# Performance work log

Hardware: AMD Instinct MI355X
Metric: run time of the kernel (lower is better)

Reference implementation:

```python
import jax, jax.numpy as jnp
import numpy as np

VOCAB = 10000
EMB = 256
FILTERS = 256
KS = [2, 3, 4]
NUM_LABELS = 6
B, L = 4, 256


def _conv1d_same(x, w, b, k):
    # x: [B, C, L], w: [O, I, k] -> [B, O, L]; torch 'same' pad: left=(k-1)//2
    pad_l = (k - 1) // 2
    pad_r = (k - 1) - pad_l
    y = jax.lax.conv_general_dilated(
        x, w, window_strides=(1,), padding=[(pad_l, pad_r)],
        dimension_numbers=('NCH', 'OIH', 'NCH'))
    return y + b[None, :, None]


def setup_inputs() -> dict:
    key = jax.random.key(0)
    ks = jax.random.split(key, 12)
    s = 0.02
    return {
        'input_ids': jax.random.randint(ks[0], (B, L), 0, VOCAB),
        'emb_table': jax.random.normal(ks[1], (VOCAB, EMB), jnp.float32) * s,
        'w2': jax.random.normal(ks[2], (FILTERS, EMB, 2), jnp.float32) * s,
        'b2': jax.random.normal(ks[3], (FILTERS,), jnp.float32) * s,
        'w3': jax.random.normal(ks[4], (FILTERS, EMB, 3), jnp.float32) * s,
        'b3': jax.random.normal(ks[5], (FILTERS,), jnp.float32) * s,
        'w4': jax.random.normal(ks[6], (FILTERS, EMB, 4), jnp.float32) * s,
        'b4': jax.random.normal(ks[7], (FILTERS,), jnp.float32) * s,
        'triple_w': jax.random.normal(ks[8], (NUM_LABELS, 3 * FILTERS), jnp.float32) * s,
        'triple_b': jax.random.normal(ks[9], (NUM_LABELS,), jnp.float32) * s,
        'score_w': jax.random.normal(ks[10], (1, 3 * FILTERS), jnp.float32) * s,
        'score_b': jax.random.normal(ks[11], (1,), jnp.float32) * s,
    }


def reference(input_ids, emb_table, w2, b2, w3, b3, w4, b4,
              triple_w, triple_b, score_w, score_b):
    emb = emb_table[input_ids]              # [B, L, E]
    x = jnp.transpose(emb, (0, 2, 1))       # [B, E, L]
    outs = [_conv1d_same(x, w, b, k) for (w, b, k)
            in ((w2, b2, 2), (w3, b3, 3), (w4, b4, 4))]
    out = jnp.concatenate(outs, axis=1)     # [B, 3F, L]
    out = jnp.transpose(out, (0, 2, 1))     # [B, L, K], K = 3F
    # dropout is identity in eval mode
    pair = jnp.einsum('bik,bjk->bijk', out, out)          # [B, L, L, K]
    triple_logits = jnp.einsum('bijk,ck->bijc', pair, triple_w) + triple_b
    scores = jnp.einsum('bijk,ck->bijc', pair, score_w) + score_b
    scores = scores[..., 0]                 # squeeze(-1) -> [B, L, L]
    return triple_logits, scores
```

## Files before the change

kernel.cpp:

```cpp
#include <hip/hip_runtime.h>
#include <stdint.h>

#define LSEQ 256
#define EMB  256
#define K3F  768
#define SCOFF (4 * 256 * 256 * 6)

typedef short bf16x8 __attribute__((ext_vector_type(8)));
typedef float f32x4  __attribute__((ext_vector_type(4)));

__device__ __forceinline__ uint16_t f2bf(float x) {
    union { float f; uint32_t u; } c; c.f = x;
    uint32_t r = c.u + 0x7fffu + ((c.u >> 16) & 1u);
    return (uint16_t)(r >> 16);
}

__global__ __launch_bounds__(256) void k_prep(const int* __restrict__ ids,
                                              const float* __restrict__ table,
                                              const float* __restrict__ w2,
                                              const float* __restrict__ w3,
                                              const float* __restrict__ w4,
                                              uint16_t* __restrict__ embB,
                                              uint16_t* __restrict__ Wt2,
                                              uint16_t* __restrict__ Wt3,
                                              uint16_t* __restrict__ Wt4) {
    int blk = blockIdx.x, tid = threadIdx.x;
    if (blk < 32) {
        int b = blk >> 3, l0 = (blk & 7) << 5;
        int r = tid >> 3, p = tid & 7;
        int id = ids[(b << 8) + l0 + r];
        const float* src = table + (size_t)id * EMB + p * 32;
        uint16_t* dst = embB + (size_t)(b * 272 + 4 + l0 + r) * 256 + p * 32;
#pragma unroll
        for (int s = 0; s < 8; ++s) {
            float4 v = *(const float4*)(src + 4 * s);
            uint32_t lo = f2bf(v.x) | ((uint32_t)f2bf(v.y) << 16);
            uint32_t hi = f2bf(v.z) | ((uint32_t)f2bf(v.w) << 16);
            *(uint2*)(dst + 4 * s) = make_uint2(lo, hi);
        }
    } else if (blk < 36) {
        int b = blk - 32;
        int ri = tid >> 4;
        int row = ri < 4 ? ri : 256 + ri;
        int off = (tid & 15) * 16;
        uint16_t* dst = embB + (size_t)(b * 272 + row) * 256 + off;
        *(uint4*)dst = make_uint4(0, 0, 0, 0);
        *(uint4*)(dst + 8) = make_uint4(0, 0, 0, 0);
    } else {
        int n = (blk - 36) * 256 + tid;
        if (n < 131072) {
            int t = n >> 16, rem = n & 65535, c = rem >> 8, i = rem & 255;
            Wt2[n] = f2bf(w2[(c << 9) + (i << 1) + t]);
        } else if (n < 327680) {
            int m = n - 131072;
            int t = m >> 16, rem = m & 65535, c = rem >> 8, i = rem & 255;
            Wt3[m] = f2bf(w3[c * 768 + i * 3 + t]);
        } else if (n < 589824) {
            int m = n - 327680;
            int t = m >> 16, rem = m & 65535, c = rem >> 8, i = rem & 255;
            Wt4[m] = f2bf(w4[(c << 10) + (i << 2) + t]);
        }
    }
}

template <int K, int PAD>
__device__ __forceinline__ void convg_body(const uint16_t* __restrict__ Wt,
                                           const float* __restrict__ bias,
                                           const uint16_t* __restrict__ embB,
                                           const float* __restrict__ tw,
                                           const float* __restrict__ sw,
                                           uint16_t* __restrict__ VB,
                                           uint16_t* __restrict__ U,
                                           int b, int c0, int l0, int gbase,
                                           uint16_t (*As)[32][72], uint16_t (*Bs)[72],
                                           float (*twb)[32]) {
    const int tid = threadIdx.x;
    {
        int cm = tid >> 5, cc = tid & 31;
        int gch = gbase + c0 + cc;
        float v;
        if (cm < 6) v = tw[cm * K3F + gch];
        else if (cm == 6) v = sw[gch];
        else v = bias[c0 + cc];
        twb[cm][cc] = v;
    }
    const int lane = tid & 63, wave = tid >> 6;
    const int ms = wave >> 1, ns = wave & 1;
    const int m = lane & 15, q = lane >> 4;
    const int ar = tid >> 3, aseg = (tid & 7) * 8;

    f32x4 acc;
#pragma unroll
    for (int z = 0; z < 4; ++z) acc[z] = 0.f;

    for (int i0 = 0; i0 < EMB; i0 += 64) {
        __syncthreads();
#pragma unroll
        for (int t = 0; t < K; ++t) {
            const uint16_t* src = Wt + (size_t)((t * 256 + c0 + ar) * 256 + i0) + aseg;
            *(bf16x8*)&As[t][ar][aseg] = *(const bf16x8*)src;
        }
        {
            const uint16_t* src = embB + (size_t)(b * 272 + 3 + l0 + ar) * 256 + i0 + aseg;
            *(bf16x8*)&Bs[ar][aseg] = *(const bf16x8*)src;
            if (tid < 32) {
                int r2 = 32 + (tid >> 3);
                const uint16_t* s2 = embB + (size_t)(b * 272 + 3 + l0 + r2) * 256 + i0 + aseg;
                *(bf16x8*)&Bs[r2][aseg] = *(const bf16x8*)s2;
            }
        }
        __syncthreads();
#pragma unroll
        for (int t = 0; t < K; ++t) {
#pragma unroll
            for (int kh = 0; kh < 64; kh += 32) {
                bf16x8 afr = *(const bf16x8*)&As[t][ms * 16 + m][kh + q * 8];
                bf16x8 bfr = *(const bf16x8*)&Bs[ns * 16 + m + t - PAD + 1][kh + q * 8];
                acc = __builtin_amdgcn_mfma_f32_16x16x32_bf16(afr, bfr, acc, 0, 0, 0);
            }
        }
    }
    __syncthreads();
    float (*Cs)[36] = (float(*)[36])As;
#pragma unroll
    for (int rg = 0; rg < 4; ++rg)
        Cs[ms * 16 + q * 4 + rg][ns * 16 + m] = acc[rg];
    __syncthreads();
    const int l = tid >> 3, cs = (tid & 7) * 4;
    float vals[4];
#pragma unroll
    for (int v = 0; v < 4; ++v) vals[v] = Cs[cs + v][l] + twb[7][cs + v];
    union { uint16_t h[4]; uint32_t d[2]; } pk;
#pragma unroll
    for (int v = 0; v < 4; ++v) pk.h[v] = f2bf(vals[v]);
    uint16_t* vdst = VB + (size_t)(b * 256 + l0 + l) * K3F + gbase + c0 + cs;
    *(uint2*)vdst = *(const uint2*)pk.d;
#pragma unroll
    for (int cm = 0; cm < 7; ++cm) {
#pragma unroll
        for (int v = 0; v < 4; ++v) pk.h[v] = f2bf(vals[v] * twb[cm][cs + v]);
        uint16_t* udst = U + (size_t)((b * 7 + cm) * 256 + l0 + l) * K3F + gbase + c0 + cs;
        *(uint2*)udst = *(const uint2*)pk.d;
    }
}

__global__ __launch_bounds__(256, 2) void k_convg(const uint16_t* __restrict__ Wt2,
                                                  const uint16_t* __restrict__ Wt3,
                                                  const uint16_t* __restrict__ Wt4,
                                                  const float* __restrict__ b2,
                                                  const float* __restrict__ b3,
                                                  const float* __restrict__ b4,
                                                  const uint16_t* __restrict__ embB,
                                                  const float* __restrict__ tw,
                                                  const float* __restrict__ sw,
                                                  uint16_t* __restrict__ VB,
                                                  uint16_t* __restrict__ U) {
    __shared__ uint16_t As[4][32][72];
    __shared__ uint16_t Bs[36][72];
    __shared__ float twb[8][32];
    int blk = blockIdx.x;
    int b = blk & 3, rest = blk >> 2;
    int g = rest >> 6, rr = rest & 63;
    int c0 = (rr >> 3) * 32, l0 = (rr & 7) * 32;
    if (g == 0)      convg_body<2, 0>(Wt2, b2, embB, tw, sw, VB, U, b, c0, l0, 0,   As, Bs, twb);
    else if (g == 1) convg_body<3, 1>(Wt3, b3, embB, tw, sw, VB, U, b, c0, l0, 256, As, Bs, twb);
    else             convg_body<4, 1>(Wt4, b4, embB, tw, sw, VB, U, b, c0, l0, 512, As, Bs, twb);
}

__global__ __launch_bounds__(256, 4) void k_pairc(const uint16_t* __restrict__ U,
                                                  const uint16_t* __restrict__ VB,
                                                  const float* __restrict__ tb,
                                                  const float* __restrict__ sb,
                                                  float* __restrict__ dout) {
    __shared__ uint16_t T[64][136];
    int blk = blockIdx.x;
    int jt = blk & 7, it = (blk >> 3) & 7;
    int c = (blk >> 6) % 7, b = blk / 448;
    int i0 = it * 32, j0 = jt * 32;
    int tid = threadIdx.x;
    int lane = tid & 63, wave = tid >> 6;
    int ms = wave >> 1, ns = wave & 1;
    int m = lane & 15, q = lane >> 4;
    int rs = tid >> 2, off = (tid & 3) * 32;

    const uint16_t* srcA = U + (size_t)((b * 7 + c) * 256 + i0 + rs) * K3F + off;
    const uint16_t* srcB = VB + (size_t)(b * 256 + j0 + (rs - 32)) * K3F + off;
    const uint16_t* src = (rs < 32) ? srcA : srcB;

    f32x4 acc;
#pragma unroll
    for (int z = 0; z < 4; ++z) acc[z] = 0.f;

    for (int kc = 0; kc < K3F; kc += 128) {
        __syncthreads();
#pragma unroll
        for (int s = 0; s < 4; ++s)
            *(bf16x8*)&T[rs][off + s * 8] = *(const bf16x8*)(src + kc + s * 8);
        __syncthreads();
#pragma unroll
        for (int kh = 0; kh < 4; ++kh) {
            bf16x8 afr = *(const bf16x8*)&T[ms * 16 + m][kh * 32 + q * 8];
            bf16x8 bfr = *(const bf16x8*)&T[32 + ns * 16 + m][kh * 32 + q * 8];
            acc = __builtin_amdgcn_mfma_f32_16x16x32_bf16(afr, bfr, acc, 0, 0, 0);
        }
    }
    float bias = (c < 6) ? tb[c] : sb[0];
#pragma unroll
    for (int rg = 0; rg < 4; ++rg) {
        int i = i0 + ms * 16 + q * 4 + rg;
        int j = j0 + ns * 16 + m;
        float v = acc[rg] + bias;
        if (c < 6) dout[((size_t)(b * 256 + i) * 256 + j) * 6 + c] = v;
        else       dout[SCOFF + (size_t)(b * 256 + i) * 256 + j] = v;
    }
}

extern "C" void kernel_launch(void* const* d_in, const int* in_sizes, int n_in,
                              void* d_out, int out_size, void* d_ws, size_t ws_size,
                              hipStream_t stream) {
    const int*   ids   = (const int*)d_in[0];
    const float* table = (const float*)d_in[1];
    const float* w2 = (const float*)d_in[2];
    const float* b2 = (const float*)d_in[3];
    const float* w3 = (const float*)d_in[4];
    const float* b3 = (const float*)d_in[5];
    const float* w4 = (const float*)d_in[6];
    const float* b4 = (const float*)d_in[7];
    const float* tw = (const float*)d_in[8];
    const float* tb = (const float*)d_in[9];
    const float* sw = (const float*)d_in[10];
    const float* sb = (const float*)d_in[11];
    float* dout = (float*)d_out;

    uint8_t* wsb = (uint8_t*)d_ws;
    uint16_t* embB = (uint16_t*)(wsb + 0);
    uint16_t* Wt2  = (uint16_t*)(wsb + 557056);
    uint16_t* Wt3  = (uint16_t*)(wsb + 819200);
    uint16_t* Wt4  = (uint16_t*)(wsb + 1212416);
    uint16_t* VB   = (uint16_t*)(wsb + 1736704);
    uint16_t* U    = (uint16_t*)(wsb + 3309568);

    hipLaunchKernelGGL(k_prep,  dim3(2340), dim3(256), 0, stream,
                       ids, table, w2, w3, w4, embB, Wt2, Wt3, Wt4);
    hipLaunchKernelGGL(k_convg, dim3(768),  dim3(256), 0, stream,
                       Wt2, Wt3, Wt4, b2, b3, b4, embB, tw, sw, VB, U);
    hipLaunchKernelGGL(k_pairc, dim3(1792), dim3(256), 0, stream, U, VB, tb, sb, dout);
}
```

Before: 113.4 us.

## Fuse embedding gather and weight bf16 conversion into conv kernel

New measurement: 116.0 us. 2.3% more time.

```diff
diff --git a/kernel.cpp b/kernel.cpp
--- a/kernel.cpp
+++ b/kernel.cpp
@@ -15,58 +15,11 @@
     return (uint16_t)(r >> 16);
 }
 
-__global__ __launch_bounds__(256) void k_prep(const int* __restrict__ ids,
-                                              const float* __restrict__ table,
-                                              const float* __restrict__ w2,
-                                              const float* __restrict__ w3,
-                                              const float* __restrict__ w4,
-                                              uint16_t* __restrict__ embB,
-                                              uint16_t* __restrict__ Wt2,
-                                              uint16_t* __restrict__ Wt3,
-                                              uint16_t* __restrict__ Wt4) {
-    int blk = blockIdx.x, tid = threadIdx.x;
-    if (blk < 32) {
-        int b = blk >> 3, l0 = (blk & 7) << 5;
-        int r = tid >> 3, p = tid & 7;
-        int id = ids[(b << 8) + l0 + r];
-        const float* src = table + (size_t)id * EMB + p * 32;
-        uint16_t* dst = embB + (size_t)(b * 272 + 4 + l0 + r) * 256 + p * 32;
-#pragma unroll
-        for (int s = 0; s < 8; ++s) {
-            float4 v = *(const float4*)(src + 4 * s);
-            uint32_t lo = f2bf(v.x) | ((uint32_t)f2bf(v.y) << 16);
-            uint32_t hi = f2bf(v.z) | ((uint32_t)f2bf(v.w) << 16);
-            *(uint2*)(dst + 4 * s) = make_uint2(lo, hi);
-        }
-    } else if (blk < 36) {
-        int b = blk - 32;
-        int ri = tid >> 4;
-        int row = ri < 4 ? ri : 256 + ri;
-        int off = (tid & 15) * 16;
-        uint16_t* dst = embB + (size_t)(b * 272 + row) * 256 + off;
-        *(uint4*)dst = make_uint4(0, 0, 0, 0);
-        *(uint4*)(dst + 8) = make_uint4(0, 0, 0, 0);
-    } else {
-        int n = (blk - 36) * 256 + tid;
-        if (n < 131072) {
-            int t = n >> 16, rem = n & 65535, c = rem >> 8, i = rem & 255;
-            Wt2[n] = f2bf(w2[(c << 9) + (i << 1) + t]);
-        } else if (n < 327680) {
-            int m = n - 131072;
-            int t = m >> 16, rem = m & 65535, c = rem >> 8, i = rem & 255;
-            Wt3[m] = f2bf(w3[c * 768 + i * 3 + t]);
-        } else if (n < 589824) {
-            int m = n - 327680;
-            int t = m >> 16, rem = m & 65535, c = rem >> 8, i = rem & 255;
-            Wt4[m] = f2bf(w4[(c << 10) + (i << 2) + t]);
-        }
-    }
-}
-
 template <int K, int PAD>
-__device__ __forceinline__ void convg_body(const uint16_t* __restrict__ Wt,
+__device__ __forceinline__ void conv2_body(const float* __restrict__ w,
                                            const float* __restrict__ bias,
-                                           const uint16_t* __restrict__ embB,
+                                           const int* __restrict__ ids,
+                                           const float* __restrict__ table,
                                            const float* __restrict__ tw,
                                            const float* __restrict__ sw,
                                            uint16_t* __restrict__ VB,
@@ -87,7 +40,15 @@
     const int lane = tid & 63, wave = tid >> 6;
     const int ms = wave >> 1, ns = wave & 1;
     const int m = lane & 15, q = lane >> 4;
-    const int ar = tid >> 3, aseg = (tid & 7) * 8;
+    const int ar = tid >> 3, pb = (tid & 7) * 8;
+
+    const int l1 = l0 - 1 + ar;
+    const bool v1 = (l1 >= 0) && (l1 < LSEQ);
+    const float* trow1 = v1 ? table + (size_t)ids[(b << 8) + (v1 ? l1 : 0)] * EMB : nullptr;
+    const int r2 = 32 + (tid >> 3);
+    const int l2 = l0 - 1 + r2;
+    const bool v2 = (tid < 32) && (l2 < LSEQ);
+    const float* trow2 = v2 ? table + (size_t)ids[(b << 8) + (v2 ? l2 : 0)] * EMB : nullptr;
 
     f32x4 acc;
 #pragma unroll
@@ -97,17 +58,40 @@
         __syncthreads();
 #pragma unroll
         for (int t = 0; t < K; ++t) {
-            const uint16_t* src = Wt + (size_t)((t * 256 + c0 + ar) * 256 + i0) + aseg;
-            *(bf16x8*)&As[t][ar][aseg] = *(const bf16x8*)src;
+            const float* wsrc = w + (size_t)(c0 + ar) * (EMB * K) + (size_t)(i0 + pb) * K + t;
+            union { uint16_t h[8]; uint32_t d[4]; } pk;
+#pragma unroll
+            for (int j = 0; j < 8; ++j) pk.h[j] = f2bf(wsrc[j * K]);
+            *(uint2*)&As[t][ar][pb]     = make_uint2(pk.d[0], pk.d[1]);
+            *(uint2*)&As[t][ar][pb + 4] = make_uint2(pk.d[2], pk.d[3]);
         }
         {
-            const uint16_t* src = embB + (size_t)(b * 272 + 3 + l0 + ar) * 256 + i0 + aseg;
-            *(bf16x8*)&Bs[ar][aseg] = *(const bf16x8*)src;
-            if (tid < 32) {
-                int r2 = 32 + (tid >> 3);
-                const uint16_t* s2 = embB + (size_t)(b * 272 + 3 + l0 + r2) * 256 + i0 + aseg;
-                *(bf16x8*)&Bs[r2][aseg] = *(const bf16x8*)s2;
+            union { uint16_t h[8]; uint32_t d[4]; } pk;
+            if (v1) {
+                float4 a = *(const float4*)(trow1 + i0 + pb);
+                float4 c = *(const float4*)(trow1 + i0 + pb + 4);
+                pk.h[0] = f2bf(a.x); pk.h[1] = f2bf(a.y); pk.h[2] = f2bf(a.z); pk.h[3] = f2bf(a.w);
+                pk.h[4] = f2bf(c.x); pk.h[5] = f2bf(c.y); pk.h[6] = f2bf(c.z); pk.h[7] = f2bf(c.w);
+            } else {
+#pragma unroll
+                for (int j = 0; j < 4; ++j) pk.d[j] = 0u;
             }
+            *(uint2*)&Bs[ar][pb]     = make_uint2(pk.d[0], pk.d[1]);
+            *(uint2*)&Bs[ar][pb + 4] = make_uint2(pk.d[2], pk.d[3]);
+        }
+        if (tid < 32) {
+            union { uint16_t h[8]; uint32_t d[4]; } pk;
+            if (v2) {
+                float4 a = *(const float4*)(trow2 + i0 + pb);
+                float4 c = *(const float4*)(trow2 + i0 + pb + 4);
+                pk.h[0] = f2bf(a.x); pk.h[1] = f2bf(a.y); pk.h[2] = f2bf(a.z); pk.h[3] = f2bf(a.w);
+                pk.h[4] = f2bf(c.x); pk.h[5] = f2bf(c.y); pk.h[6] = f2bf(c.z); pk.h[7] = f2bf(c.w);
+            } else {
+#pragma unroll
+                for (int j = 0; j < 4; ++j) pk.d[j] = 0u;
+            }
+            *(uint2*)&Bs[r2][pb]     = make_uint2(pk.d[0], pk.d[1]);
+            *(uint2*)&Bs[r2][pb + 4] = make_uint2(pk.d[2], pk.d[3]);
         }
         __syncthreads();
 #pragma unroll
@@ -144,13 +128,14 @@
     }
 }
 
-__global__ __launch_bounds__(256, 2) void k_convg(const uint16_t* __restrict__ Wt2,
-                                                  const uint16_t* __restrict__ Wt3,
-                                                  const uint16_t* __restrict__ Wt4,
+__global__ __launch_bounds__(256, 2) void k_conv2(const float* __restrict__ w2,
                                                   const float* __restrict__ b2,
+                                                  const float* __restrict__ w3,
                                                   const float* __restrict__ b3,
+                                                  const float* __restrict__ w4,
                                                   const float* __restrict__ b4,
-                                                  const uint16_t* __restrict__ embB,
+                                                  const int* __restrict__ ids,
+                                                  const float* __restrict__ table,
                                                   const float* __restrict__ tw,
                                                   const float* __restrict__ sw,
                                                   uint16_t* __restrict__ VB,
@@ -162,9 +147,9 @@
     int b = blk & 3, rest = blk >> 2;
     int g = rest >> 6, rr = rest & 63;
     int c0 = (rr >> 3) * 32, l0 = (rr & 7) * 32;
-    if (g == 0)      convg_body<2, 0>(Wt2, b2, embB, tw, sw, VB, U, b, c0, l0, 0,   As, Bs, twb);
-    else if (g == 1) convg_body<3, 1>(Wt3, b3, embB, tw, sw, VB, U, b, c0, l0, 256, As, Bs, twb);
-    else             convg_body<4, 1>(Wt4, b4, embB, tw, sw, VB, U, b, c0, l0, 512, As, Bs, twb);
+    if (g == 0)      conv2_body<2, 0>(w2, b2, ids, table, tw, sw, VB, U, b, c0, l0, 0,   As, Bs, twb);
+    else if (g == 1) conv2_body<3, 1>(w3, b3, ids, table, tw, sw, VB, U, b, c0, l0, 256, As, Bs, twb);
+    else             conv2_body<4, 1>(w4, b4, ids, table, tw, sw, VB, U, b, c0, l0, 512, As, Bs, twb);
 }
 
 __global__ __launch_bounds__(256, 4) void k_pairc(const uint16_t* __restrict__ U,
@@ -233,16 +218,10 @@
     float* dout = (float*)d_out;
 
     uint8_t* wsb = (uint8_t*)d_ws;
-    uint16_t* embB = (uint16_t*)(wsb + 0);
-    uint16_t* Wt2  = (uint16_t*)(wsb + 557056);
-    uint16_t* Wt3  = (uint16_t*)(wsb + 819200);
-    uint16_t* Wt4  = (uint16_t*)(wsb + 1212416);
-    uint16_t* VB   = (uint16_t*)(wsb + 1736704);
-    uint16_t* U    = (uint16_t*)(wsb + 3309568);
-
-    hipLaunchKernelGGL(k_prep,  dim3(2340), dim3(256), 0, stream,
-                       ids, table, w2, w3, w4, embB, Wt2, Wt3, Wt4);
-    hipLaunchKernelGGL(k_convg, dim3(768),  dim3(256), 0, stream,
-                       Wt2, Wt3, Wt4, b2, b3, b4, embB, tw, sw, VB, U);
+    uint16_t* VB = (uint16_t*)(wsb + 0);
+    uint16_t* U  = (uint16_t*)(wsb + 1572864);
+
+    hipLaunchKernelGGL(k_conv2, dim3(768), dim3(256), 0, stream,
+                       w2, b2, w3, b3, w4, b4, ids, table, tw, sw, VB, U);
     hipLaunchKernelGGL(k_pairc, dim3(1792), dim3(256), 0, stream, U, VB, tb, sb, dout);
 }
```

## Widen pair-kernel tile to 32x64, vectorize weight prep, reorder workspace

Applied to the files above, without the earlier changes.

New measurement: 109.3 us, median of 2. -3.6%, faster.

```diff
diff --git a/kernel.cpp b/kernel.cpp
--- a/kernel.cpp
+++ b/kernel.cpp
@@ -48,17 +48,26 @@
         *(uint4*)(dst + 8) = make_uint4(0, 0, 0, 0);
     } else {
         int n = (blk - 36) * 256 + tid;
-        if (n < 131072) {
-            int t = n >> 16, rem = n & 65535, c = rem >> 8, i = rem & 255;
-            Wt2[n] = f2bf(w2[(c << 9) + (i << 1) + t]);
-        } else if (n < 327680) {
+        if (n < 65536) {
+            int c = n >> 8, i = n & 255;
+            float2 v = *(const float2*)(w2 + (c << 9) + (i << 1));
+            Wt2[c * 256 + i]         = f2bf(v.x);
+            Wt2[65536 + c * 256 + i] = f2bf(v.y);
+        } else if (n < 131072) {
+            int m = n - 65536;
+            int c = m >> 8, i = m & 255;
+            const float* s = w3 + c * 768 + i * 3;
+#pragma unroll
+            for (int t = 0; t < 3; ++t)
+                Wt3[t * 65536 + c * 256 + i] = f2bf(s[t]);
+        } else {
             int m = n - 131072;
-            int t = m >> 16, rem = m & 65535, c = rem >> 8, i = rem & 255;
-            Wt3[m] = f2bf(w3[c * 768 + i * 3 + t]);
-        } else if (n < 589824) {
-            int m = n - 327680;
-            int t = m >> 16, rem = m & 65535, c = rem >> 8, i = rem & 255;
-            Wt4[m] = f2bf(w4[(c << 10) + (i << 2) + t]);
+            int c = m >> 8, i = m & 255;
+            float4 v = *(const float4*)(w4 + (c << 10) + (i << 2));
+            Wt4[c * 256 + i]              = f2bf(v.x);
+            Wt4[65536 + c * 256 + i]      = f2bf(v.y);
+            Wt4[2 * 65536 + c * 256 + i]  = f2bf(v.z);
+            Wt4[3 * 65536 + c * 256 + i]  = f2bf(v.w);
         }
     }
 }
@@ -167,52 +176,63 @@
     else             convg_body<4, 1>(Wt4, b4, embB, tw, sw, VB, U, b, c0, l0, 512, As, Bs, twb);
 }
 
-__global__ __launch_bounds__(256, 4) void k_pairc(const uint16_t* __restrict__ U,
-                                                  const uint16_t* __restrict__ VB,
-                                                  const float* __restrict__ tb,
-                                                  const float* __restrict__ sb,
-                                                  float* __restrict__ dout) {
-    __shared__ uint16_t T[64][136];
+__global__ __launch_bounds__(256, 4) void k_pairc2(const uint16_t* __restrict__ U,
+                                                   const uint16_t* __restrict__ VB,
+                                                   const float* __restrict__ tb,
+                                                   const float* __restrict__ sb,
+                                                   float* __restrict__ dout) {
+    __shared__ uint16_t T[96][136];
     int blk = blockIdx.x;
-    int jt = blk & 7, it = (blk >> 3) & 7;
-    int c = (blk >> 6) % 7, b = blk / 448;
-    int i0 = it * 32, j0 = jt * 32;
+    int b = blk & 3, it = (blk >> 2) & 7;
+    int rest = blk >> 5;
+    int c = rest % 7, jp = rest / 7;
+    int i0 = it * 32, j0 = jp * 64;
     int tid = threadIdx.x;
     int lane = tid & 63, wave = tid >> 6;
-    int ms = wave >> 1, ns = wave & 1;
+    int iw = wave >> 1, jw = wave & 1;
     int m = lane & 15, q = lane >> 4;
-    int rs = tid >> 2, off = (tid & 3) * 32;
-
-    const uint16_t* srcA = U + (size_t)((b * 7 + c) * 256 + i0 + rs) * K3F + off;
-    const uint16_t* srcB = VB + (size_t)(b * 256 + j0 + (rs - 32)) * K3F + off;
-    const uint16_t* src = (rs < 32) ? srcA : srcB;
-
-    f32x4 acc;
-#pragma unroll
-    for (int z = 0; z < 4; ++z) acc[z] = 0.f;
+    int rr = tid >> 3, seg = (tid & 7) * 16;
+
+    const uint16_t* srcp[3];
+    srcp[0] = U + (size_t)((b * 7 + c) * 256 + i0 + rr) * K3F + seg;
+    srcp[1] = VB + (size_t)(b * 256 + j0 + rr) * K3F + seg;
+    srcp[2] = VB + (size_t)(b * 256 + j0 + 32 + rr) * K3F + seg;
+
+    f32x4 acc[2];
+#pragma unroll
+    for (int n = 0; n < 2; ++n)
+#pragma unroll
+        for (int z = 0; z < 4; ++z) acc[n][z] = 0.f;
 
     for (int kc = 0; kc < K3F; kc += 128) {
         __syncthreads();
 #pragma unroll
-        for (int s = 0; s < 4; ++s)
-            *(bf16x8*)&T[rs][off + s * 8] = *(const bf16x8*)(src + kc + s * 8);
+        for (int p = 0; p < 3; ++p) {
+            const uint16_t* s = srcp[p] + kc;
+            *(bf16x8*)&T[p * 32 + rr][seg]     = *(const bf16x8*)s;
+            *(bf16x8*)&T[p * 32 + rr][seg + 8] = *(const bf16x8*)(s + 8);
+        }
         __syncthreads();
 #pragma unroll
         for (int kh = 0; kh < 4; ++kh) {
-            bf16x8 afr = *(const bf16x8*)&T[ms * 16 + m][kh * 32 + q * 8];
-            bf16x8 bfr = *(const bf16x8*)&T[32 + ns * 16 + m][kh * 32 + q * 8];
-            acc = __builtin_amdgcn_mfma_f32_16x16x32_bf16(afr, bfr, acc, 0, 0, 0);
+            bf16x8 afr  = *(const bf16x8*)&T[iw * 16 + m][kh * 32 + q * 8];
+            bf16x8 bfr0 = *(const bf16x8*)&T[32 + jw * 32 + m][kh * 32 + q * 8];
+            bf16x8 bfr1 = *(const bf16x8*)&T[32 + jw * 32 + 16 + m][kh * 32 + q * 8];
+            acc[0] = __builtin_amdgcn_mfma_f32_16x16x32_bf16(afr, bfr0, acc[0], 0, 0, 0);
+            acc[1] = __builtin_amdgcn_mfma_f32_16x16x32_bf16(afr, bfr1, acc[1], 0, 0, 0);
         }
     }
     float bias = (c < 6) ? tb[c] : sb[0];
 #pragma unroll
-    for (int rg = 0; rg < 4; ++rg) {
-        int i = i0 + ms * 16 + q * 4 + rg;
-        int j = j0 + ns * 16 + m;
-        float v = acc[rg] + bias;
-        if (c < 6) dout[((size_t)(b * 256 + i) * 256 + j) * 6 + c] = v;
-        else       dout[SCOFF + (size_t)(b * 256 + i) * 256 + j] = v;
-    }
+    for (int n = 0; n < 2; ++n)
+#pragma unroll
+        for (int rg = 0; rg < 4; ++rg) {
+            int i = i0 + iw * 16 + q * 4 + rg;
+            int j = j0 + jw * 32 + n * 16 + m;
+            float v = acc[n][rg] + bias;
+            if (c < 6) dout[((size_t)(b * 256 + i) * 256 + j) * 6 + c] = v;
+            else       dout[SCOFF + (size_t)(b * 256 + i) * 256 + j] = v;
+        }
 }
 
 extern "C" void kernel_launch(void* const* d_in, const int* in_sizes, int n_in,
@@ -233,16 +253,16 @@
     float* dout = (float*)d_out;
 
     uint8_t* wsb = (uint8_t*)d_ws;
-    uint16_t* embB = (uint16_t*)(wsb + 0);
-    uint16_t* Wt2  = (uint16_t*)(wsb + 557056);
-    uint16_t* Wt3  = (uint16_t*)(wsb + 819200);
-    uint16_t* Wt4  = (uint16_t*)(wsb + 1212416);
-    uint16_t* VB   = (uint16_t*)(wsb + 1736704);
-    uint16_t* U    = (uint16_t*)(wsb + 3309568);
-
-    hipLaunchKernelGGL(k_prep,  dim3(2340), dim3(256), 0, stream,
+    uint16_t* VB   = (uint16_t*)(wsb + 0);
+    uint16_t* U    = (uint16_t*)(wsb + 1572864);
+    uint16_t* embB = (uint16_t*)(wsb + 12582912);
+    uint16_t* Wt2  = (uint16_t*)(wsb + 13139968);
+    uint16_t* Wt3  = (uint16_t*)(wsb + 13402112);
+    uint16_t* Wt4  = (uint16_t*)(wsb + 13795328);
+
+    hipLaunchKernelGGL(k_prep,   dim3(804), dim3(256), 0, stream,
                        ids, table, w2, w3, w4, embB, Wt2, Wt3, Wt4);
-    hipLaunchKernelGGL(k_convg, dim3(768),  dim3(256), 0, stream,
+    hipLaunchKernelGGL(k_convg,  dim3(768), dim3(256), 0, stream,
                        Wt2, Wt3, Wt4, b2, b3, b4, embB, tw, sw, VB, U);
-    hipLaunchKernelGGL(k_pairc, dim3(1792), dim3(256), 0, stream, U, VB, tb, sb, dout);
-}
+    hipLaunchKernelGGL(k_pairc2, dim3(896), dim3(256), 0, stream, U, VB, tb, sb, dout);
+}
```
